# Performance work log

Measured on AMD Instinct MI355X. Metric: run time of the kernel, lower is better.

Reference implementation:

```python
import jax, jax.numpy as jnp
import numpy as np

B, N, IN_DIM, OUT_DIM, H = 8, 1024, 256, 256, 4
HD = OUT_DIM // H  # head_dim = 64
NEG = -1e9
EPS = 1e-5


def setup_inputs() -> dict:
    key = jax.random.key(0)
    ks = jax.random.split(key, 9)
    h = jax.random.normal(ks[0], (B, N, IN_DIM), dtype=jnp.float32)
    adj = jax.random.randint(ks[1], (N, N), 0, 2, dtype=jnp.int32)
    adj = adj.at[jnp.arange(N), jnp.arange(N)].set(1)  # self loops so no empty rows
    s = 1.0 / np.sqrt(IN_DIM)
    W = jax.random.uniform(ks[2], (H, IN_DIM, HD), jnp.float32, -s, s)
    sa = 1.0 / np.sqrt(2 * HD)
    a1 = jax.random.uniform(ks[3], (H, HD), jnp.float32, -sa, sa)
    a2 = jax.random.uniform(ks[4], (H, HD), jnp.float32, -sa, sa)
    sp = 1.0 / np.sqrt(OUT_DIM)
    proj_w = jax.random.uniform(ks[5], (OUT_DIM, OUT_DIM), jnp.float32, -sp, sp)
    proj_b = jax.random.uniform(ks[6], (OUT_DIM,), jnp.float32, -sp, sp)
    gamma = jnp.ones((OUT_DIM,), jnp.float32)
    beta = jnp.zeros((OUT_DIM,), jnp.float32)
    return {"h": h, "adj": adj, "W": W, "a1": a1, "a2": a2,
            "proj_w": proj_w, "proj_b": proj_b, "gamma": gamma, "beta": beta}


def reference(h, adj, W, a1, a2, proj_w, proj_b, gamma, beta):
    # Wh: [B,H,N,HD]
    Wh = jnp.einsum('bni,hid->bhnd', h, W)
    # Decompose a([Wh_i || Wh_j]) = a1.Wh_i + a2.Wh_j (same math as concat+linear)
    si = jnp.einsum('bhnd,hd->bhn', Wh, a1)  # [B,H,N]
    sj = jnp.einsum('bhnd,hd->bhn', Wh, a2)
    e = jax.nn.leaky_relu(si[:, :, :, None] + sj[:, :, None, :], 0.2)  # [B,H,N,N]
    mask = (adj == 0)  # [N,N]
    e = jnp.where(mask[None, None], NEG, e)
    alpha = jax.nn.softmax(e, axis=-1)
    out = jnp.einsum('bhnm,bhmd->bhnd', alpha, Wh)  # [B,H,N,HD]
    h_multi = out.transpose(0, 2, 1, 3).reshape(B, N, OUT_DIM)  # concat heads
    h_out = jnp.einsum('bnd,od->bno', h_multi, proj_w) + proj_b
    h_out = h_out + h  # residual (in_dim == out_dim)
    mu = jnp.mean(h_out, axis=-1, keepdims=True)
    var = jnp.mean(jnp.square(h_out - mu), axis=-1, keepdims=True)
    return (h_out - mu) * jax.lax.rsqrt(var + EPS) * gamma + beta
```

## Files before the change

kernel.cpp:

```cpp
#include <hip/hip_runtime.h>
#include <hip/hip_bf16.h>

#define BB 8
#define NN 1024
#define IN_DIM 256
#define OUT_DIM 256
#define NH 4
#define HD 64
#define TN 16
#define TM 128
#define PSTR 136

typedef __attribute__((ext_vector_type(8))) short short8;
typedef __attribute__((ext_vector_type(4))) short short4e;
typedef __attribute__((ext_vector_type(4))) float floatx4;
typedef __attribute__((ext_vector_type(4))) int intx4;

__global__ __launch_bounds__(256) void prep_kernel(
    const float* __restrict__ W,
    const float* __restrict__ a1, const float* __restrict__ a2,
    const float* __restrict__ proj_w, const int* __restrict__ adj,
    __hip_bfloat16* __restrict__ WTb,
    __hip_bfloat16* __restrict__ pwb,
    __hip_bfloat16* __restrict__ wab,
    unsigned* __restrict__ adjm)
{
    int blk = blockIdx.x, t = threadIdx.x;
    if (blk < 16) {
        int o = blk * 16 + (t >> 4);
        int hh = o >> 6, d = o & 63;
        #pragma unroll
        for (int kk = 0; kk < 16; ++kk) {
            int k = (t & 15) + 16 * kk;
            WTb[(size_t)o * 256 + k] = __float2bfloat16(W[((size_t)hh * 256 + k) * 64 + d]);
        }
    } else if (blk < 32) {
        size_t base = (size_t)(blk - 16) * 4096 + t * 16;
        #pragma unroll
        for (int k = 0; k < 16; k += 4) {
            floatx4 v = *(const floatx4*)(proj_w + base + k);
            alignas(8) __hip_bfloat16 tmp[4];
            #pragma unroll
            for (int j = 0; j < 4; ++j) tmp[j] = __float2bfloat16(v[j]);
            *(short4e*)(pwb + base + k) = *(const short4e*)tmp;
        }
    } else if (blk < 40) {
        int r = blk - 32;
        int hh = r & 3;
        const float* av = (r < 4 ? a1 : a2) + hh * HD;
        const float* wrow = W + ((size_t)hh * 256 + t) * HD;
        float s = 0.f;
        #pragma unroll 8
        for (int d = 0; d < HD; ++d) s += wrow[d] * av[d];
        wab[(size_t)r * 256 + t] = __float2bfloat16(s);
        wab[(size_t)(r + 8) * 256 + t] = __float2bfloat16(0.f);
    } else {
        int bp = blk - 40;
        int n = bp * 8 + (t >> 5);
        int wd = t & 31;
        const int* arow = adj + (size_t)n * NN + wd * 32;
        unsigned bits = 0;
        #pragma unroll
        for (int j4 = 0; j4 < 8; ++j4) {
            intx4 v = *(const intx4*)(arow + j4 * 4);
            #pragma unroll
            for (int j = 0; j < 4; ++j) if (v[j] != 0) bits |= (1u << (j4 * 4 + j));
        }
        adjm[(size_t)n * 32 + wd] = bits;
    }
}

__global__ __launch_bounds__(256) void wh_mfma_kernel(
    const float* __restrict__ h,
    const __hip_bfloat16* __restrict__ WTb,
    const __hip_bfloat16* __restrict__ wab,
    __hip_bfloat16* __restrict__ WhT,
    float* __restrict__ si, float* __restrict__ sj)
{
    int t = threadIdx.x;
    int w = t >> 6, l = t & 63;
    int rl = l & 15, q = l >> 4;
    int r0 = blockIdx.x * 16;

    short8 af[8];
    const float* Arow = h + (size_t)(r0 + rl) * 256 + q * 8;
    #pragma unroll
    for (int k0 = 0; k0 < 8; ++k0) {
        floatx4 v0 = *(const floatx4*)(Arow + k0 * 32);
        floatx4 v1 = *(const floatx4*)(Arow + k0 * 32 + 4);
        short8 a;
        #pragma unroll
        for (int j = 0; j < 4; ++j) {
            a[j]     = (short)(__bfloat16_as_ushort(__float2bfloat16(v0[j])));
            a[j + 4] = (short)(__bfloat16_as_ushort(__float2bfloat16(v1[j])));
        }
        af[k0] = a;
    }

    int bb = r0 >> 10;
    int n0 = (r0 & 1023) + q * 4;

    #pragma unroll
    for (int j = 0; j < 4; ++j) {
        int ct = w + j * 4;
        const __hip_bfloat16* Brow = WTb + (size_t)(ct * 16 + rl) * 256 + q * 8;
        floatx4 acc = {0.f, 0.f, 0.f, 0.f};
        #pragma unroll
        for (int k0 = 0; k0 < 8; ++k0) {
            short8 bf = *(const short8*)(Brow + k0 * 32);
            acc = __builtin_amdgcn_mfma_f32_16x16x32_bf16(af[k0], bf, acc, 0, 0, 0);
        }
        int o = ct * 16 + rl;
        int hh = o >> 6, d = o & 63;
        alignas(8) __hip_bfloat16 tmp[4];
        #pragma unroll
        for (int i = 0; i < 4; ++i) tmp[i] = __float2bfloat16(acc[i]);
        *(short4e*)(WhT + ((size_t)(bb * NH + hh) * HD + d) * NN + n0) = *(const short4e*)tmp;
    }

    if (w == 0) {
        const __hip_bfloat16* Brow = wab + (size_t)rl * 256 + q * 8;
        floatx4 acc = {0.f, 0.f, 0.f, 0.f};
        #pragma unroll
        for (int k0 = 0; k0 < 8; ++k0) {
            short8 bf = *(const short8*)(Brow + k0 * 32);
            acc = __builtin_amdgcn_mfma_f32_16x16x32_bf16(af[k0], bf, acc, 0, 0, 0);
        }
        if (rl < 8) {
            int hh = rl & 3;
            float* dst = (rl < 4 ? si : sj) + ((size_t)(bb * NH + hh)) * NN + n0;
            *(floatx4*)dst = acc;
        }
    }
}

__global__ __launch_bounds__(256) void attn_kernel(
    const unsigned* __restrict__ adjm,
    const __hip_bfloat16* __restrict__ WhT,
    const float* __restrict__ si,
    const float* __restrict__ sj,
    __hip_bfloat16* __restrict__ hmb)
{
    int bx = blockIdx.x;
    int bh = bx >> 6;
    int n0 = (bx & 63) * TN;
    int t = threadIdx.x;

    __shared__ __align__(16) __hip_bfloat16 p_lds[TN * PSTR];
    __shared__ float rinv[TN];

    int r = t >> 4, c = t & 15;
    int n = n0 + r;
    float sii = si[(size_t)bh * NN + n];
    const float* sjr = sj + (size_t)bh * NN;
    const unsigned* amrow = adjm + (size_t)n * 32;

    int w = t >> 6, l = t & 63;
    int rl = l & 15, q = l >> 4;
    int d0 = w * 16;
    const __hip_bfloat16* Bb = WhT + ((size_t)bh * HD + d0 + rl) * NN + q * 8;
    const __hip_bfloat16* Ab = p_lds + (size_t)rl * PSTR + q * 8;

    float lsum = 0.f;
    floatx4 acc = {0.f, 0.f, 0.f, 0.f};

    for (int m0 = 0; m0 < NN; m0 += TM) {
        floatx4 s0 = *(const floatx4*)(sjr + m0 + c * 8);
        floatx4 s1 = *(const floatx4*)(sjr + m0 + c * 8 + 4);
        unsigned wv = amrow[(m0 >> 5) + (c >> 2)];
        unsigned sh = (c & 3) * 8;
        alignas(16) __hip_bfloat16 tmp[8];
        #pragma unroll
        for (int k = 0; k < 8; ++k) {
            float x = sii + (k < 4 ? s0[k] : s1[k - 4]);
            x = x > 0.f ? x : 0.2f * x;
            x = ((wv >> (sh + k)) & 1u) ? x : -1e9f;
            float pv = __expf(x);
            lsum += pv;
            tmp[k] = __float2bfloat16(pv);
        }
        *(short8*)(p_lds + (size_t)r * PSTR + c * 8) = *(const short8*)tmp;
        __syncthreads();
        #pragma unroll
        for (int ks = 0; ks < 4; ++ks) {
            short8 af = *(const short8*)(Ab + ks * 32);
            short8 bf = *(const short8*)(Bb + m0 + ks * 32);
            acc = __builtin_amdgcn_mfma_f32_16x16x32_bf16(af, bf, acc, 0, 0, 0);
        }
        __syncthreads();
    }

    #pragma unroll
    for (int off = 1; off < 16; off <<= 1) lsum += __shfl_xor(lsum, off, 64);
    if (c == 0) rinv[r] = 1.f / lsum;
    __syncthreads();

    int b = bh >> 2, hhh = bh & 3;
    #pragma unroll
    for (int i = 0; i < 4; ++i) {
        int nr = q * 4 + i;
        float v = acc[i] * rinv[nr];
        hmb[((size_t)(b * NN) + n0 + nr) * OUT_DIM + hhh * HD + d0 + rl] = __float2bfloat16(v);
    }
}

__global__ __launch_bounds__(256) void proj_ln_kernel(
    const __hip_bfloat16* __restrict__ hmb,
    const float* __restrict__ h,
    const __hip_bfloat16* __restrict__ pwb,
    const float* __restrict__ proj_b,
    const float* __restrict__ gamma,
    const float* __restrict__ beta,
    float* __restrict__ out)
{
    int t = threadIdx.x;
    int w = t >> 6, l = t & 63;
    int rl = l & 15, q = l >> 4;
    int r0 = blockIdx.x * 16;

    __shared__ float red[2][4][16];

    short8 af[8];
    const __hip_bfloat16* Arow = hmb + (size_t)(r0 + rl) * 256 + q * 8;
    #pragma unroll
    for (int k0 = 0; k0 < 8; ++k0) af[k0] = *(const short8*)(Arow + k0 * 32);

    floatx4 acc[4];
    #pragma unroll
    for (int j = 0; j < 4; ++j) {
        int ct = w + j * 4;
        const __hip_bfloat16* Brow = pwb + (size_t)(ct * 16 + rl) * 256 + q * 8;
        floatx4 a = {0.f, 0.f, 0.f, 0.f};
        #pragma unroll
        for (int k0 = 0; k0 < 8; ++k0) {
            short8 bf = *(const short8*)(Brow + k0 * 32);
            a = __builtin_amdgcn_mfma_f32_16x16x32_bf16(af[k0], bf, a, 0, 0, 0);
        }
        acc[j] = a;
    }

    float ps[4] = {0.f, 0.f, 0.f, 0.f};
    #pragma unroll
    for (int j = 0; j < 4; ++j) {
        int col = (w + j * 4) * 16 + rl;
        float pb = proj_b[col];
        #pragma unroll
        for (int i = 0; i < 4; ++i) {
            float v = acc[j][i] + pb + h[(size_t)(r0 + q * 4 + i) * 256 + col];
            acc[j][i] = v;
            ps[i] += v;
        }
    }
    #pragma unroll
    for (int i = 0; i < 4; ++i) {
        float s = ps[i];
        #pragma unroll
        for (int off = 1; off < 16; off <<= 1) s += __shfl_xor(s, off, 64);
        ps[i] = s;
    }
    if (rl == 0) {
        for (int i = 0; i < 4; ++i) red[0][w][q * 4 + i] = ps[i];
    }
    __syncthreads();
    float mu[4];
    #pragma unroll
    for (int i = 0; i < 4; ++i) {
        int row = q * 4 + i;
        mu[i] = (red[0][0][row] + red[0][1][row] + red[0][2][row] + red[0][3][row]) * (1.f / 256.f);
    }

    float vs[4] = {0.f, 0.f, 0.f, 0.f};
    #pragma unroll
    for (int j = 0; j < 4; ++j) {
        #pragma unroll
        for (int i = 0; i < 4; ++i) { float cv = acc[j][i] - mu[i]; vs[i] += cv * cv; }
    }
    #pragma unroll
    for (int i = 0; i < 4; ++i) {
        float s = vs[i];
        #pragma unroll
        for (int off = 1; off < 16; off <<= 1) s += __shfl_xor(s, off, 64);
        vs[i] = s;
    }
    if (rl == 0) {
        for (int i = 0; i < 4; ++i) red[1][w][q * 4 + i] = vs[i];
    }
    __syncthreads();
    float rs[4];
    #pragma unroll
    for (int i = 0; i < 4; ++i) {
        int row = q * 4 + i;
        float var = (red[1][0][row] + red[1][1][row] + red[1][2][row] + red[1][3][row]) * (1.f / 256.f);
        rs[i] = rsqrtf(var + 1e-5f);
    }

    #pragma unroll
    for (int j = 0; j < 4; ++j) {
        int col = (w + j * 4) * 16 + rl;
        float g = gamma[col], be = beta[col];
        #pragma unroll
        for (int i = 0; i < 4; ++i)
            out[(size_t)(r0 + q * 4 + i) * 256 + col] = (acc[j][i] - mu[i]) * rs[i] * g + be;
    }
}

extern "C" void kernel_launch(void* const* d_in, const int* in_sizes, int n_in,
                              void* d_out, int out_size, void* d_ws, size_t ws_size,
                              hipStream_t stream) {
    const float* h      = (const float*)d_in[0];
    const int*   adj    = (const int*)d_in[1];
    const float* W      = (const float*)d_in[2];
    const float* a1     = (const float*)d_in[3];
    const float* a2     = (const float*)d_in[4];
    const float* proj_w = (const float*)d_in[5];
    const float* proj_b = (const float*)d_in[6];
    const float* gamma  = (const float*)d_in[7];
    const float* beta   = (const float*)d_in[8];
    float* out = (float*)d_out;

    char* ws = (char*)d_ws;
    __hip_bfloat16* WhT = (__hip_bfloat16*)ws;                    ws += (size_t)BB*NH*HD*NN*2;
    __hip_bfloat16* hmb = (__hip_bfloat16*)ws;                    ws += (size_t)BB*NN*OUT_DIM*2;
    __hip_bfloat16* WTb = (__hip_bfloat16*)ws;                    ws += 256*256*2;
    __hip_bfloat16* pwb = (__hip_bfloat16*)ws;                    ws += 256*256*2;
    __hip_bfloat16* wab = (__hip_bfloat16*)ws;                    ws += 16*256*2;
    float* si = (float*)ws;                                       ws += (size_t)BB*NH*NN*4;
    float* sj = (float*)ws;                                       ws += (size_t)BB*NH*NN*4;
    unsigned* adjm = (unsigned*)ws;                               ws += (size_t)NN*32*4;

    prep_kernel<<<168, 256, 0, stream>>>(W, a1, a2, proj_w, adj, WTb, pwb, wab, adjm);
    wh_mfma_kernel<<<512, 256, 0, stream>>>(h, WTb, wab, WhT, si, sj);
    attn_kernel<<<BB * NH * (NN / TN), 256, 0, stream>>>(adjm, WhT, si, sj, hmb);
    proj_ln_kernel<<<512, 256, 0, stream>>>(hmb, h, pwb, proj_b, gamma, beta, out);
}
```

Measured before the change: 142.0 us.

## Fuse prep into Wh kernel and fuse attention with projection+LayerNorm

Cuts the pipeline from four launches to two. The prep work (proj_w bf16 conversion, adjacency bitmask) is folded into the Wh kernel as extra blocks. W is now read and converted to bf16 inside the MFMA loop, and si/sj are computed by reducing Wh against a1/a2 through shuffles and LDS instead of a separate weight product. Attention now has one block per 16 rows covering all four heads, one wave per head, with all 64 head dims per wave and no block barriers. The head outputs are staged in LDS and fed straight into the projection+LayerNorm epilogue, which removes the hmb round trip and two launches. The cost is strided, uncoalesced fp32 reads of W repeated in every Wh block, and only 512 attention blocks, each doing more work per wave.

```diff
diff --git a/kernel.cpp b/kernel.cpp
--- a/kernel.cpp
+++ b/kernel.cpp
@@ -1,86 +1,63 @@
 #include <hip/hip_runtime.h>
 #include <hip/hip_bf16.h>
 
-#define BB 8
 #define NN 1024
-#define IN_DIM 256
-#define OUT_DIM 256
-#define NH 4
-#define HD 64
-#define TN 16
-#define TM 128
-#define PSTR 136
 
 typedef __attribute__((ext_vector_type(8))) short short8;
 typedef __attribute__((ext_vector_type(4))) short short4e;
 typedef __attribute__((ext_vector_type(4))) float floatx4;
 typedef __attribute__((ext_vector_type(4))) int intx4;
 
-__global__ __launch_bounds__(256) void prep_kernel(
-    const float* __restrict__ W,
+static __device__ __forceinline__ short bfb(float x) {
+    return (short)__bfloat16_as_ushort(__float2bfloat16(x));
+}
+
+__global__ __launch_bounds__(256) void wh_kernel(
+    const float* __restrict__ h, const float* __restrict__ W,
     const float* __restrict__ a1, const float* __restrict__ a2,
     const float* __restrict__ proj_w, const int* __restrict__ adj,
-    __hip_bfloat16* __restrict__ WTb,
+    __hip_bfloat16* __restrict__ WhT,
+    float* __restrict__ si, float* __restrict__ sj,
     __hip_bfloat16* __restrict__ pwb,
-    __hip_bfloat16* __restrict__ wab,
     unsigned* __restrict__ adjm)
 {
     int blk = blockIdx.x, t = threadIdx.x;
-    if (blk < 16) {
-        int o = blk * 16 + (t >> 4);
-        int hh = o >> 6, d = o & 63;
-        #pragma unroll
-        for (int kk = 0; kk < 16; ++kk) {
-            int k = (t & 15) + 16 * kk;
-            WTb[(size_t)o * 256 + k] = __float2bfloat16(W[((size_t)hh * 256 + k) * 64 + d]);
-        }
-    } else if (blk < 32) {
-        size_t base = (size_t)(blk - 16) * 4096 + t * 16;
-        #pragma unroll
-        for (int k = 0; k < 16; k += 4) {
-            floatx4 v = *(const floatx4*)(proj_w + base + k);
-            alignas(8) __hip_bfloat16 tmp[4];
-            #pragma unroll
-            for (int j = 0; j < 4; ++j) tmp[j] = __float2bfloat16(v[j]);
-            *(short4e*)(pwb + base + k) = *(const short4e*)tmp;
-        }
-    } else if (blk < 40) {
-        int r = blk - 32;
-        int hh = r & 3;
-        const float* av = (r < 4 ? a1 : a2) + hh * HD;
-        const float* wrow = W + ((size_t)hh * 256 + t) * HD;
-        float s = 0.f;
-        #pragma unroll 8
-        for (int d = 0; d < HD; ++d) s += wrow[d] * av[d];
-        wab[(size_t)r * 256 + t] = __float2bfloat16(s);
-        wab[(size_t)(r + 8) * 256 + t] = __float2bfloat16(0.f);
-    } else {
-        int bp = blk - 40;
-        int n = bp * 8 + (t >> 5);
-        int wd = t & 31;
-        const int* arow = adj + (size_t)n * NN + wd * 32;
-        unsigned bits = 0;
-        #pragma unroll
-        for (int j4 = 0; j4 < 8; ++j4) {
-            intx4 v = *(const intx4*)(arow + j4 * 4);
-            #pragma unroll
-            for (int j = 0; j < 4; ++j) if (v[j] != 0) bits |= (1u << (j4 * 4 + j));
-        }
-        adjm[(size_t)n * 32 + wd] = bits;
-    }
-}
-
-__global__ __launch_bounds__(256) void wh_mfma_kernel(
-    const float* __restrict__ h,
-    const __hip_bfloat16* __restrict__ WTb,
-    const __hip_bfloat16* __restrict__ wab,
-    __hip_bfloat16* __restrict__ WhT,
-    float* __restrict__ si, float* __restrict__ sj)
-{
-    int t = threadIdx.x;
+
+    if (blk >= 512) {
+        if (blk < 528) {
+            size_t base = (size_t)(blk - 512) * 4096 + (size_t)t * 16;
+            #pragma unroll
+            for (int k = 0; k < 16; k += 4) {
+                floatx4 v = *(const floatx4*)(proj_w + base + k);
+                alignas(8) __hip_bfloat16 tmp[4];
+                #pragma unroll
+                for (int j = 0; j < 4; ++j) tmp[j] = __float2bfloat16(v[j]);
+                *(short4e*)(pwb + base + k) = *(const short4e*)tmp;
+            }
+        } else {
+            int n = (blk - 528) * 8 + (t >> 5);
+            int wd = t & 31;
+            const int* arow = adj + (size_t)n * NN + wd * 32;
+            unsigned bits = 0;
+            #pragma unroll
+            for (int j4 = 0; j4 < 8; ++j4) {
+                intx4 v = *(const intx4*)(arow + j4 * 4);
+                #pragma unroll
+                for (int j = 0; j < 4; ++j) if (v[j] != 0) bits |= (1u << (j4 * 4 + j));
+            }
+            adjm[(size_t)n * 32 + wd] = bits;
+        }
+        return;
+    }
+
     int w = t >> 6, l = t & 63;
     int rl = l & 15, q = l >> 4;
-    int r0 = blockIdx.x * 16;
+    int r0 = blk * 16;
+    int bb = r0 >> 10;
+    int n0 = r0 & 1023;
+
+    __shared__ float redsi[4][4][16];
+    __shared__ float redsj[4][4][16];
 
     short8 af[8];
     const float* Arow = h + (size_t)(r0 + rl) * 256 + q * 8;
@@ -90,142 +67,150 @@
         floatx4 v1 = *(const floatx4*)(Arow + k0 * 32 + 4);
         short8 a;
         #pragma unroll
-        for (int j = 0; j < 4; ++j) {
-            a[j]     = (short)(__bfloat16_as_ushort(__float2bfloat16(v0[j])));
-            a[j + 4] = (short)(__bfloat16_as_ushort(__float2bfloat16(v1[j])));
-        }
+        for (int j = 0; j < 4; ++j) { a[j] = bfb(v0[j]); a[j + 4] = bfb(v1[j]); }
         af[k0] = a;
     }
 
-    int bb = r0 >> 10;
-    int n0 = (r0 & 1023) + q * 4;
+    float a1v[4], a2v[4];
+    #pragma unroll
+    for (int j = 0; j < 4; ++j) {
+        a1v[j] = a1[j * 64 + w * 16 + rl];
+        a2v[j] = a2[j * 64 + w * 16 + rl];
+    }
 
     #pragma unroll
     for (int j = 0; j < 4; ++j) {
         int ct = w + j * 4;
-        const __hip_bfloat16* Brow = WTb + (size_t)(ct * 16 + rl) * 256 + q * 8;
+        const float* Wb = W + (size_t)(ct >> 2) * 16384 + (ct & 3) * 16 + rl;
         floatx4 acc = {0.f, 0.f, 0.f, 0.f};
         #pragma unroll
         for (int k0 = 0; k0 < 8; ++k0) {
-            short8 bf = *(const short8*)(Brow + k0 * 32);
-            acc = __builtin_amdgcn_mfma_f32_16x16x32_bf16(af[k0], bf, acc, 0, 0, 0);
-        }
-        int o = ct * 16 + rl;
-        int hh = o >> 6, d = o & 63;
+            short8 bfr;
+            #pragma unroll
+            for (int jj = 0; jj < 8; ++jj)
+                bfr[jj] = bfb(Wb[(size_t)(k0 * 32 + q * 8 + jj) * 64]);
+            acc = __builtin_amdgcn_mfma_f32_16x16x32_bf16(af[k0], bfr, acc, 0, 0, 0);
+        }
+
         alignas(8) __hip_bfloat16 tmp[4];
         #pragma unroll
         for (int i = 0; i < 4; ++i) tmp[i] = __float2bfloat16(acc[i]);
-        *(short4e*)(WhT + ((size_t)(bb * NH + hh) * HD + d) * NN + n0) = *(const short4e*)tmp;
-    }
+        *(short4e*)(WhT + ((size_t)(bb * 4 + j) * 64 + w * 16 + rl) * NN + n0 + q * 4) =
+            *(const short4e*)tmp;
+
+        #pragma unroll
+        for (int i = 0; i < 4; ++i) {
+            float p1 = acc[i] * a1v[j];
+            float p2 = acc[i] * a2v[j];
+            #pragma unroll
+            for (int off = 1; off < 16; off <<= 1) {
+                p1 += __shfl_xor(p1, off, 64);
+                p2 += __shfl_xor(p2, off, 64);
+            }
+            if (rl == 0) { redsi[w][j][q * 4 + i] = p1; redsj[w][j][q * 4 + i] = p2; }
+        }
+    }
+    __syncthreads();
 
     if (w == 0) {
-        const __hip_bfloat16* Brow = wab + (size_t)rl * 256 + q * 8;
-        floatx4 acc = {0.f, 0.f, 0.f, 0.f};
-        #pragma unroll
-        for (int k0 = 0; k0 < 8; ++k0) {
-            short8 bf = *(const short8*)(Brow + k0 * 32);
-            acc = __builtin_amdgcn_mfma_f32_16x16x32_bf16(af[k0], bf, acc, 0, 0, 0);
-        }
-        if (rl < 8) {
-            int hh = rl & 3;
-            float* dst = (rl < 4 ? si : sj) + ((size_t)(bb * NH + hh)) * NN + n0;
-            *(floatx4*)dst = acc;
-        }
+        int head = l >> 4, row = l & 15;
+        float s = redsi[0][head][row] + redsi[1][head][row] + redsi[2][head][row] + redsi[3][head][row];
+        si[(size_t)(bb * 4 + head) * NN + n0 + row] = s;
+    } else if (w == 1) {
+        int head = l >> 4, row = l & 15;
+        float s = redsj[0][head][row] + redsj[1][head][row] + redsj[2][head][row] + redsj[3][head][row];
+        sj[(size_t)(bb * 4 + head) * NN + n0 + row] = s;
     }
 }
 
-__global__ __launch_bounds__(256) void attn_kernel(
+__global__ __launch_bounds__(256) void attn_proj_kernel(
     const unsigned* __restrict__ adjm,
     const __hip_bfloat16* __restrict__ WhT,
-    const float* __restrict__ si,
-    const float* __restrict__ sj,
-    __hip_bfloat16* __restrict__ hmb)
-{
-    int bx = blockIdx.x;
-    int bh = bx >> 6;
-    int n0 = (bx & 63) * TN;
-    int t = threadIdx.x;
-
-    __shared__ __align__(16) __hip_bfloat16 p_lds[TN * PSTR];
-    __shared__ float rinv[TN];
-
-    int r = t >> 4, c = t & 15;
-    int n = n0 + r;
-    float sii = si[(size_t)bh * NN + n];
-    const float* sjr = sj + (size_t)bh * NN;
-    const unsigned* amrow = adjm + (size_t)n * 32;
-
-    int w = t >> 6, l = t & 63;
-    int rl = l & 15, q = l >> 4;
-    int d0 = w * 16;
-    const __hip_bfloat16* Bb = WhT + ((size_t)bh * HD + d0 + rl) * NN + q * 8;
-    const __hip_bfloat16* Ab = p_lds + (size_t)rl * PSTR + q * 8;
-
-    float lsum = 0.f;
-    floatx4 acc = {0.f, 0.f, 0.f, 0.f};
-
-    for (int m0 = 0; m0 < NN; m0 += TM) {
-        floatx4 s0 = *(const floatx4*)(sjr + m0 + c * 8);
-        floatx4 s1 = *(const floatx4*)(sjr + m0 + c * 8 + 4);
-        unsigned wv = amrow[(m0 >> 5) + (c >> 2)];
-        unsigned sh = (c & 3) * 8;
-        alignas(16) __hip_bfloat16 tmp[8];
-        #pragma unroll
-        for (int k = 0; k < 8; ++k) {
-            float x = sii + (k < 4 ? s0[k] : s1[k - 4]);
-            x = x > 0.f ? x : 0.2f * x;
-            x = ((wv >> (sh + k)) & 1u) ? x : -1e9f;
-            float pv = __expf(x);
-            lsum += pv;
-            tmp[k] = __float2bfloat16(pv);
-        }
-        *(short8*)(p_lds + (size_t)r * PSTR + c * 8) = *(const short8*)tmp;
-        __syncthreads();
-        #pragma unroll
-        for (int ks = 0; ks < 4; ++ks) {
-            short8 af = *(const short8*)(Ab + ks * 32);
-            short8 bf = *(const short8*)(Bb + m0 + ks * 32);
-            acc = __builtin_amdgcn_mfma_f32_16x16x32_bf16(af, bf, acc, 0, 0, 0);
-        }
-        __syncthreads();
-    }
-
-    #pragma unroll
-    for (int off = 1; off < 16; off <<= 1) lsum += __shfl_xor(lsum, off, 64);
-    if (c == 0) rinv[r] = 1.f / lsum;
-    __syncthreads();
-
-    int b = bh >> 2, hhh = bh & 3;
-    #pragma unroll
-    for (int i = 0; i < 4; ++i) {
-        int nr = q * 4 + i;
-        float v = acc[i] * rinv[nr];
-        hmb[((size_t)(b * NN) + n0 + nr) * OUT_DIM + hhh * HD + d0 + rl] = __float2bfloat16(v);
-    }
-}
-
-__global__ __launch_bounds__(256) void proj_ln_kernel(
-    const __hip_bfloat16* __restrict__ hmb,
+    const float* __restrict__ si, const float* __restrict__ sj,
+    const __hip_bfloat16* __restrict__ pwb,
     const float* __restrict__ h,
-    const __hip_bfloat16* __restrict__ pwb,
-    const float* __restrict__ proj_b,
-    const float* __restrict__ gamma,
+    const float* __restrict__ proj_b, const float* __restrict__ gamma,
     const float* __restrict__ beta,
     float* __restrict__ out)
 {
-    int t = threadIdx.x;
+    int blk = blockIdx.x, t = threadIdx.x;
     int w = t >> 6, l = t & 63;
     int rl = l & 15, q = l >> 4;
-    int r0 = blockIdx.x * 16;
-
+    int b = blk >> 6, n0 = (blk & 63) * 16;
+    int bh = b * 4 + w;
+    int r0 = blk * 16;
+
+    __shared__ __align__(16) __hip_bfloat16 p_lds[4][16 * 136];
+    __shared__ __align__(16) __hip_bfloat16 hm_stage[16][264];
+    __shared__ float rinvs[4][16];
     __shared__ float red[2][4][16];
 
-    short8 af[8];
-    const __hip_bfloat16* Arow = hmb + (size_t)(r0 + rl) * 256 + q * 8;
-    #pragma unroll
-    for (int k0 = 0; k0 < 8; ++k0) af[k0] = *(const short8*)(Arow + k0 * 32);
-
-    floatx4 acc[4];
+    int r = l >> 2, cg = l & 3;
+    float sii = si[(size_t)bh * NN + n0 + r];
+    const float* sjr = sj + (size_t)bh * NN;
+    const unsigned* amrow = adjm + (size_t)(n0 + r) * 32;
+
+    __hip_bfloat16* pt = &p_lds[w][0];
+    const __hip_bfloat16* Ab = pt + rl * 136 + q * 8;
+    const __hip_bfloat16* Bbase = WhT + ((size_t)bh * 64 + rl) * NN + q * 8;
+
+    float lsum = 0.f;
+    floatx4 acc[4] = { {0,0,0,0}, {0,0,0,0}, {0,0,0,0}, {0,0,0,0} };
+
+    for (int m0 = 0; m0 < NN; m0 += 128) {
+        int mb = m0 + cg * 32;
+        unsigned bits = amrow[mb >> 5];
+        alignas(16) __hip_bfloat16 tmp[32];
+        #pragma unroll
+        for (int c4 = 0; c4 < 8; ++c4) {
+            floatx4 s4 = *(const floatx4*)(sjr + mb + c4 * 4);
+            #pragma unroll
+            for (int k = 0; k < 4; ++k) {
+                float x = sii + s4[k];
+                x = x > 0.f ? x : 0.2f * x;
+                x = ((bits >> (c4 * 4 + k)) & 1u) ? x : -1e9f;
+                float pv = __expf(x);
+                lsum += pv;
+                tmp[c4 * 4 + k] = __float2bfloat16(pv);
+            }
+        }
+        {
+            short8* dst = (short8*)(pt + r * 136 + cg * 32);
+            const short8* srcv = (const short8*)tmp;
+            dst[0] = srcv[0]; dst[1] = srcv[1]; dst[2] = srcv[2]; dst[3] = srcv[3];
+        }
+        #pragma unroll
+        for (int ks = 0; ks < 4; ++ks) {
+            short8 afr = *(const short8*)(Ab + ks * 32);
+            #pragma unroll
+            for (int dt = 0; dt < 4; ++dt) {
+                short8 bfr = *(const short8*)(Bbase + (size_t)dt * 16 * NN + m0 + ks * 32);
+                acc[dt] = __builtin_amdgcn_mfma_f32_16x16x32_bf16(afr, bfr, acc[dt], 0, 0, 0);
+            }
+        }
+    }
+
+    lsum += __shfl_xor(lsum, 1, 64);
+    lsum += __shfl_xor(lsum, 2, 64);
+    if (cg == 0) rinvs[w][r] = 1.f / lsum;
+    float riv[4];
+    #pragma unroll
+    for (int i = 0; i < 4; ++i) riv[i] = rinvs[w][q * 4 + i];
+
+    #pragma unroll
+    for (int dt = 0; dt < 4; ++dt) {
+        #pragma unroll
+        for (int i = 0; i < 4; ++i)
+            hm_stage[q * 4 + i][w * 64 + dt * 16 + rl] = __float2bfloat16(acc[dt][i] * riv[i]);
+    }
+    __syncthreads();
+
+    short8 paf[8];
+    const __hip_bfloat16* Arow2 = &hm_stage[rl][0] + q * 8;
+    #pragma unroll
+    for (int k0 = 0; k0 < 8; ++k0) paf[k0] = *(const short8*)(Arow2 + k0 * 32);
+
+    floatx4 pacc[4];
     #pragma unroll
     for (int j = 0; j < 4; ++j) {
         int ct = w + j * 4;
@@ -233,10 +218,10 @@
         floatx4 a = {0.f, 0.f, 0.f, 0.f};
         #pragma unroll
         for (int k0 = 0; k0 < 8; ++k0) {
-            short8 bf = *(const short8*)(Brow + k0 * 32);
-            a = __builtin_amdgcn_mfma_f32_16x16x32_bf16(af[k0], bf, a, 0, 0, 0);
-        }
-        acc[j] = a;
+            short8 bfr = *(const short8*)(Brow + k0 * 32);
+            a = __builtin_amdgcn_mfma_f32_16x16x32_bf16(paf[k0], bfr, a, 0, 0, 0);
+        }
+        pacc[j] = a;
     }
 
     float ps[4] = {0.f, 0.f, 0.f, 0.f};
@@ -246,8 +231,8 @@
         float pb = proj_b[col];
         #pragma unroll
         for (int i = 0; i < 4; ++i) {
-            float v = acc[j][i] + pb + h[(size_t)(r0 + q * 4 + i) * 256 + col];
-            acc[j][i] = v;
+            float v = pacc[j][i] + pb + h[(size_t)(r0 + q * 4 + i) * 256 + col];
+            pacc[j][i] = v;
             ps[i] += v;
         }
     }
@@ -273,7 +258,7 @@
     #pragma unroll
     for (int j = 0; j < 4; ++j) {
         #pragma unroll
-        for (int i = 0; i < 4; ++i) { float cv = acc[j][i] - mu[i]; vs[i] += cv * cv; }
+        for (int i = 0; i < 4; ++i) { float cv = pacc[j][i] - mu[i]; vs[i] += cv * cv; }
     }
     #pragma unroll
     for (int i = 0; i < 4; ++i) {
@@ -293,14 +278,13 @@
         float var = (red[1][0][row] + red[1][1][row] + red[1][2][row] + red[1][3][row]) * (1.f / 256.f);
         rs[i] = rsqrtf(var + 1e-5f);
     }
-
     #pragma unroll
     for (int j = 0; j < 4; ++j) {
         int col = (w + j * 4) * 16 + rl;
         float g = gamma[col], be = beta[col];
         #pragma unroll
         for (int i = 0; i < 4; ++i)
-            out[(size_t)(r0 + q * 4 + i) * 256 + col] = (acc[j][i] - mu[i]) * rs[i] * g + be;
+            out[(size_t)(r0 + q * 4 + i) * 256 + col] = (pacc[j][i] - mu[i]) * rs[i] * g + be;
     }
 }
 
@@ -319,17 +303,12 @@
     float* out = (float*)d_out;
 
     char* ws = (char*)d_ws;
-    __hip_bfloat16* WhT = (__hip_bfloat16*)ws;                    ws += (size_t)BB*NH*HD*NN*2;
-    __hip_bfloat16* hmb = (__hip_bfloat16*)ws;                    ws += (size_t)BB*NN*OUT_DIM*2;
-    __hip_bfloat16* WTb = (__hip_bfloat16*)ws;                    ws += 256*256*2;
-    __hip_bfloat16* pwb = (__hip_bfloat16*)ws;                    ws += 256*256*2;
-    __hip_bfloat16* wab = (__hip_bfloat16*)ws;                    ws += 16*256*2;
-    float* si = (float*)ws;                                       ws += (size_t)BB*NH*NN*4;
-    float* sj = (float*)ws;                                       ws += (size_t)BB*NH*NN*4;
-    unsigned* adjm = (unsigned*)ws;                               ws += (size_t)NN*32*4;
-
-    prep_kernel<<<168, 256, 0, stream>>>(W, a1, a2, proj_w, adj, WTb, pwb, wab, adjm);
-    wh_mfma_kernel<<<512, 256, 0, stream>>>(h, WTb, wab, WhT, si, sj);
-    attn_kernel<<<BB * NH * (NN / TN), 256, 0, stream>>>(adjm, WhT, si, sj, hmb);
-    proj_ln_kernel<<<512, 256, 0, stream>>>(hmb, h, pwb, proj_b, gamma, beta, out);
+    __hip_bfloat16* WhT = (__hip_bfloat16*)ws;   ws += (size_t)32 * 64 * NN * 2;
+    __hip_bfloat16* pwb = (__hip_bfloat16*)ws;   ws += 256 * 256 * 2;
+    float* si = (float*)ws;                      ws += (size_t)32 * NN * 4;
+    float* sj = (float*)ws;                      ws += (size_t)32 * NN * 4;
+    unsigned* adjm = (unsigned*)ws;              ws += (size_t)NN * 32 * 4;
+
+    wh_kernel<<<656, 256, 0, stream>>>(h, W, a1, a2, proj_w, adj, WhT, si, sj, pwb, adjm);
+    attn_proj_kernel<<<512, 256, 0, stream>>>(adjm, WhT, si, sj, pwb, h, proj_b, gamma, beta, out);
 }
```

After: 147.4 us. +3.8%, slower.
